# Kernel tuning notes

Measured on AMD Instinct MI355X. Metric: run time of the kernel, lower is better.

The kernel has to match this reference:

```python
import jax, jax.numpy as jnp
import numpy as np

B, S, D = 2, 2048, 4096
NH, NKV, HD = 32, 8, 128
NREP = NH // NKV

def setup_inputs() -> dict:
    key = jax.random.key(0)
    ks = jax.random.split(key, 7)
    sd = 0.02
    return {
        "x": jax.random.normal(ks[0], (B, S, D), dtype=jnp.float32),
        "freqs_cos": jnp.cos(jnp.outer(jnp.arange(S, dtype=jnp.float32), 1.0 / (10000.0 ** (jnp.arange(0, HD, 2, dtype=jnp.float32) / HD)))),
        "freqs_sin": jnp.sin(jnp.outer(jnp.arange(S, dtype=jnp.float32), 1.0 / (10000.0 ** (jnp.arange(0, HD, 2, dtype=jnp.float32) / HD)))),
        "wq": jax.random.normal(ks[1], (D, NH * HD), dtype=jnp.float32) * sd,
        "wk": jax.random.normal(ks[2], (D, NKV * HD), dtype=jnp.float32) * sd,
        "wv": jax.random.normal(ks[3], (D, NKV * HD), dtype=jnp.float32) * sd,
        "wo": jax.random.normal(ks[4], (NH * HD, D), dtype=jnp.float32) * sd,
    }

def _rope(t, cos, sin):
    # t: [b, s, h, hd]; cos/sin: [s, hd/2]
    tr = t.reshape(*t.shape[:-1], -1, 2)
    r, i = tr[..., 0], tr[..., 1]
    c = cos[None, :, None, :]
    s = sin[None, :, None, :]
    out_r = r * c - i * s
    out_i = r * s + i * c
    return jnp.stack([out_r, out_i], axis=-1).reshape(t.shape)

def reference(x, freqs_cos, freqs_sin, wq, wk, wv, wo):
    b, s, _ = x.shape
    xq = (x @ wq).reshape(b, s, NH, HD)
    xk = (x @ wk).reshape(b, s, NKV, HD)
    xv = (x @ wv).reshape(b, s, NKV, HD)
    xq = _rope(xq, freqs_cos, freqs_sin)
    xk = _rope(xk, freqs_cos, freqs_sin)
    # GQA via grouped einsum (equivalent to repeat_kv + SDPA)
    q = xq.transpose(0, 2, 1, 3).reshape(b, NKV, NREP, s, HD)  # [b,g,r,s,d]
    k = xk.transpose(0, 2, 1, 3)  # [b,g,t,d]
    v = xv.transpose(0, 2, 1, 3)
    scale = 1.0 / jnp.sqrt(jnp.float32(HD))
    scores = jnp.einsum('bgrsd,bgtd->bgrst', q, k) * scale
    mask = jnp.where(jnp.triu(jnp.ones((s, s), dtype=bool), 1), -jnp.inf, 0.0).astype(scores.dtype)
    probs = jax.nn.softmax(scores + mask, axis=-1)
    out = jnp.einsum('bgrst,bgtd->bgrsd', probs, v)
    out = out.reshape(b, NH, s, HD).transpose(0, 2, 1, 3).reshape(b, s, NH * HD)
    return out @ wo
```

## Files before the change

kernel.cpp:

```cpp
#include <hip/hip_runtime.h>
#include <hip/hip_bf16.h>
#include <math.h>

typedef __bf16 bf16_t;
typedef __bf16 bf16x4 __attribute__((ext_vector_type(4)));
typedef __bf16 bf16x8 __attribute__((ext_vector_type(8)));
typedef float  f32x4  __attribute__((ext_vector_type(4)));

#define B_   2
#define S_   2048
#define D_   4096
#define NH_  32
#define NKV_ 8
#define HD_  128
#define NREP_ 4
#define QKVN 6144

static __device__ __forceinline__ void gload_lds16(const bf16_t* g, bf16_t* l) {
  __builtin_amdgcn_global_load_lds(
      (const __attribute__((address_space(1))) void*)g,
      (__attribute__((address_space(3))) void*)l, 16, 0, 0);
}

__global__ void convert_f32_bf16(const float* __restrict__ in, bf16_t* __restrict__ out,
                                 size_t n8) {
  size_t i = (size_t)blockIdx.x * blockDim.x + threadIdx.x;
  if (i >= n8) return;
  f32x4 a = *(const f32x4*)(in + i * 8);
  f32x4 b = *(const f32x4*)(in + i * 8 + 4);
  bf16x8 o;
  o[0] = (bf16_t)a[0]; o[1] = (bf16_t)a[1]; o[2] = (bf16_t)a[2]; o[3] = (bf16_t)a[3];
  o[4] = (bf16_t)b[0]; o[5] = (bf16_t)b[1]; o[6] = (bf16_t)b[2]; o[7] = (bf16_t)b[3];
  *(bf16x8*)(out + i * 8) = o;
}

__global__ void transpose_convert(const float* __restrict__ in, bf16_t* __restrict__ out,
                                  int R, int C) {
  __shared__ float tile[32][33];
  const int c0 = blockIdx.x * 32, r0 = blockIdx.y * 32;
  const int tc = threadIdx.x & 31, tr = threadIdx.x >> 5;
#pragma unroll
  for (int i = 0; i < 4; i++) {
    int r = tr + i * 8;
    tile[r][tc] = in[(size_t)(r0 + r) * C + c0 + tc];
  }
  __syncthreads();
#pragma unroll
  for (int i = 0; i < 4; i++) {
    int r = tr + i * 8;
    out[(size_t)(c0 + r) * R + r0 + tc] = (bf16_t)tile[tc][r];
  }
}

__global__ void transpose_v(const bf16_t* __restrict__ qkv, bf16_t* __restrict__ out) {
  __shared__ bf16_t tile[32][33];
  const int t0 = blockIdx.x * 32, d0 = blockIdx.y * 32;
  const int bg = blockIdx.z, b = bg / NKV_, g = bg % NKV_;
  const bf16_t* ibase = qkv + (size_t)b * S_ * QKVN + 5120 + g * HD_;
  bf16_t* obase = out + ((size_t)b * NKV_ + g) * (size_t)HD_ * S_;
  const int tc = threadIdx.x & 31, tr = threadIdx.x >> 5;
#pragma unroll
  for (int i = 0; i < 4; i++) {
    int t = t0 + tr + i * 8;
    tile[tr + i * 8][tc] = ibase[(size_t)t * QKVN + d0 + tc];
  }
  __syncthreads();
#pragma unroll
  for (int i = 0; i < 4; i++) {
    int d = d0 + tr + i * 8;
    obase[(size_t)d * S_ + t0 + tc] = tile[tc][tr + i * 8];
  }
}

__global__ void rope_inplace(bf16_t* __restrict__ x, const float* __restrict__ cosT,
                             const float* __restrict__ sinT, int lgh, size_t nchunks) {
  size_t i = (size_t)blockIdx.x * blockDim.x + threadIdx.x;
  if (i >= nchunks) return;
  const int d8 = (int)(i & 15);
  const int h = (int)((i >> 4) & ((1u << lgh) - 1));
  const size_t pos = i >> (4 + lgh);
  const int s = (int)(pos & (S_ - 1));
  bf16_t* p = x + pos * QKVN + h * HD_ + d8 * 8;
  bf16x8 v = *(bf16x8*)p;
  f32x4 c  = *(const f32x4*)(cosT + (size_t)s * 64 + d8 * 4);
  f32x4 sn = *(const f32x4*)(sinT + (size_t)s * 64 + d8 * 4);
  bf16x8 o;
#pragma unroll
  for (int j = 0; j < 4; j++) {
    float re = (float)v[2 * j], im = (float)v[2 * j + 1];
    o[2 * j]     = (bf16_t)(re * c[j] - im * sn[j]);
    o[2 * j + 1] = (bf16_t)(re * sn[j] + im * c[j]);
  }
  *(bf16x8*)p = o;
}

template <typename OutT>
__global__ __launch_bounds__(512, 2) void gemm_nt256(const bf16_t* __restrict__ A,
                                                     const bf16_t* __restrict__ Bt,
                                                     OutT* __restrict__ C,
                                                     int M, int N, int K) {
  extern __shared__ __align__(16) bf16_t lds[];
  const int t = threadIdx.x;
  const int w = t >> 6, l = t & 63;
  const int wm = w >> 2, wn = w & 3;
  const int lr = l & 15, lg = l >> 4;

  const int nbx = gridDim.x;
  const int nwg = nbx * gridDim.y;
  const int bid = blockIdx.y * nbx + blockIdx.x;
  const int cpx = nwg >> 3;
  const int sid = (bid & 7) * cpx + (bid >> 3);
  const int n0 = (sid % nbx) * 256;
  const int m0 = (sid / nbx) * 256;

  const int srow = t >> 2;
  const int colsw = ((t & 3) * 8) ^ (((t >> 2) & 3) << 3);
  const bf16_t* Asrc0 = A  + (size_t)(m0 + srow) * K + colsw;
  const bf16_t* Asrc1 = A  + (size_t)(m0 + 128 + srow) * K + colsw;
  const bf16_t* Bsrc0 = Bt + (size_t)(n0 + srow) * K + colsw;
  const bf16_t* Bsrc1 = Bt + (size_t)(n0 + 128 + srow) * K + colsw;

  f32x4 acc[8][4];
  const f32x4 zero = {0.f, 0.f, 0.f, 0.f};
#pragma unroll
  for (int m = 0; m < 8; m++)
#pragma unroll
    for (int n = 0; n < 4; n++) acc[m][n] = zero;

  const int fo = (lg * 8) ^ ((lr & 3) << 3);

  auto STAGE = [&](int buf, int k0) {
    bf16_t* dA = lds + buf * 16384;
    bf16_t* dB = dA + 8192;
    gload_lds16(Asrc0 + k0, dA + t * 8);
    gload_lds16(Asrc1 + k0, dA + 4096 + t * 8);
    gload_lds16(Bsrc0 + k0, dB + t * 8);
    gload_lds16(Bsrc1 + k0, dB + 4096 + t * 8);
  };

  auto COMPUTE = [&](int buf) {
    const bf16_t* pA = lds + buf * 16384;
    const bf16_t* pB = pA + 8192;
    bf16x8 af[8], bfr[4];
#pragma unroll
    for (int m = 0; m < 8; m++)
      af[m] = *(const bf16x8*)(pA + (wm * 128 + m * 16 + lr) * 32 + fo);
#pragma unroll
    for (int n = 0; n < 4; n++)
      bfr[n] = *(const bf16x8*)(pB + (wn * 64 + n * 16 + lr) * 32 + fo);
    __builtin_amdgcn_s_setprio(1);
#pragma unroll
    for (int m = 0; m < 8; m++)
#pragma unroll
      for (int n = 0; n < 4; n++)
        acc[m][n] = __builtin_amdgcn_mfma_f32_16x16x32_bf16(af[m], bfr[n], acc[m][n], 0, 0, 0);
    __builtin_amdgcn_s_setprio(0);
  };

  const int KT = K >> 5;

  STAGE(0, 0);
  STAGE(1, 32);
  STAGE(2, 64);
  asm volatile("s_waitcnt vmcnt(8)" ::: "memory");
  __builtin_amdgcn_s_barrier();
  __builtin_amdgcn_sched_barrier(0);

  int kt = 0;
  for (; kt < KT - 3; ++kt) {
    STAGE((kt + 3) & 3, (kt + 3) << 5);
    COMPUTE(kt & 3);
    asm volatile("s_waitcnt vmcnt(8)" ::: "memory");
    __builtin_amdgcn_s_barrier();
    __builtin_amdgcn_sched_barrier(0);
  }
  COMPUTE(kt & 3);
  asm volatile("s_waitcnt vmcnt(4)" ::: "memory");
  __builtin_amdgcn_s_barrier();
  __builtin_amdgcn_sched_barrier(0);
  ++kt;
  COMPUTE(kt & 3);
  asm volatile("s_waitcnt vmcnt(0)" ::: "memory");
  __builtin_amdgcn_s_barrier();
  __builtin_amdgcn_sched_barrier(0);
  ++kt;
  COMPUTE(kt & 3);

#pragma unroll
  for (int m = 0; m < 8; m++)
#pragma unroll
    for (int n = 0; n < 4; n++) {
      const int row = m0 + wm * 128 + m * 16 + lg * 4;
      const int col = n0 + wn * 64 + n * 16 + lr;
#pragma unroll
      for (int r = 0; r < 4; r++) C[(size_t)(row + r) * N + col] = (OutT)acc[m][n][r];
    }
}

#define QBLK 128
#define KVBLK 64
__global__ __launch_bounds__(256, 2) void flash_attn3(const bf16_t* __restrict__ QKV,
                                                      const bf16_t* __restrict__ Vt,
                                                      bf16_t* __restrict__ O) {
  const int pair = blockIdx.x;
  const int h = blockIdx.y, b = blockIdx.z;
  const int g = h >> 2;
  const int t = threadIdx.x, w = t >> 6, l = t & 63;
  const int lr = l & 15, lg = l >> 4;

  __shared__ __align__(16) char lds[49152];
  char* Ks = lds;
  char* Vs = lds + 16384;
  char* Ps = lds + 32768 + w * 4096;

  const float scale = 0.08838834764831845f;
  const int xm = (lr & 7) << 4;

  for (int phase = 0; phase < 2; phase++) {
    const int qtile = phase ? (15 - pair) : pair;
    const int q0 = qtile * QBLK;
    const int wq = q0 + w * 32;

    bf16x8 qreg[2][4];
#pragma unroll
    for (int qt = 0; qt < 2; qt++)
#pragma unroll
      for (int kk = 0; kk < 4; kk++) {
        bf16x8 v = *(const bf16x8*)&QKV[((size_t)b * S_ + wq + qt * 16 + lr) * QKVN +
                                        h * HD_ + kk * 32 + lg * 8];
#pragma unroll
        for (int j = 0; j < 8; j++) v[j] = (bf16_t)((float)v[j] * scale);
        qreg[qt][kk] = v;
      }

    float mrun[2] = {-INFINITY, -INFINITY};
    float lrun[2] = {0.f, 0.f};
    f32x4 acc[2][8];
    const f32x4 zero = {0.f, 0.f, 0.f, 0.f};
#pragma unroll
    for (int qt = 0; qt < 2; qt++)
#pragma unroll
      for (int d = 0; d < 8; d++) acc[qt][d] = zero;

    const int nkb = (q0 + QBLK) >> 6;
    for (int kb = 0; kb < nkb; kb++) {
      const int t0 = kb * KVBLK;
      __syncthreads();
#pragma unroll
      for (int i = 0; i < 4; i++) {
        const int c = t + i * 256;
        const int row = c >> 4, sl = c & 15;
        bf16x8 kv = *(const bf16x8*)&QKV[((size_t)b * S_ + t0 + row) * QKVN + 4096 +
                                         g * HD_ + sl * 8];
        *(bf16x8*)(Ks + row * 256 + ((sl * 16) ^ ((row & 7) << 4))) = kv;
      }
#pragma unroll
      for (int i = 0; i < 4; i++) {
        const int c = t + i * 256;
        const int row = c >> 3, sl = c & 7;
        bf16x8 vv = *(const bf16x8*)&Vt[(((size_t)b * NKV_ + g) * HD_ + row) * S_ + t0 + sl * 8];
        *(bf16x8*)(Vs + row * 128 + ((sl * 16) ^ ((row & 7) << 4))) = vv;
      }
      __syncthreads();

      if (t0 > wq + 31) continue;

      f32x4 st[4][2];
#pragma unroll
      for (int n = 0; n < 4; n++) { st[n][0] = zero; st[n][1] = zero; }
#pragma unroll
      for (int kk = 0; kk < 4; kk++) {
        const int colb = (kk * 64 + lg * 16) ^ xm;
#pragma unroll
        for (int n = 0; n < 4; n++) {
          const bf16x8 ak = *(const bf16x8*)(Ks + (n * 16 + lr) * 256 + colb);
          st[n][0] = __builtin_amdgcn_mfma_f32_16x16x32_bf16(ak, qreg[0][kk], st[n][0], 0, 0, 0);
          st[n][1] = __builtin_amdgcn_mfma_f32_16x16x32_bf16(ak, qreg[1][kk], st[n][1], 0, 0, 0);
        }
      }

      const bool needmask = (t0 + KVBLK - 1 > wq);
#pragma unroll
      for (int qt = 0; qt < 2; qt++) {
        const int q = wq + qt * 16 + lr;
        if (needmask) {
#pragma unroll
          for (int n = 0; n < 4; n++)
#pragma unroll
            for (int r = 0; r < 4; r++)
              if (t0 + n * 16 + lg * 4 + r > q) st[n][qt][r] = -INFINITY;
        }
        float mx = -INFINITY;
#pragma unroll
        for (int n = 0; n < 4; n++)
#pragma unroll
          for (int r = 0; r < 4; r++) mx = fmaxf(mx, st[n][qt][r]);
        mx = fmaxf(mx, __shfl_xor(mx, 16));
        mx = fmaxf(mx, __shfl_xor(mx, 32));
        const float mnew = fmaxf(mrun[qt], mx);
        const float corr = __expf(mrun[qt] - mnew);
        mrun[qt] = mnew;
        float sum = 0.f;
        bf16x4 pk[4];
#pragma unroll
        for (int n = 0; n < 4; n++) {
#pragma unroll
          for (int r = 0; r < 4; r++) {
            const float p = __expf(st[n][qt][r] - mnew);
            sum += p;
            pk[n][r] = (bf16_t)p;
          }
        }
        sum += __shfl_xor(sum, 16);
        sum += __shfl_xor(sum, 32);
        lrun[qt] = lrun[qt] * corr + sum;
        {
          char* pbase = Ps + (qt * 16 + lr) * 128;
#pragma unroll
          for (int n = 0; n < 4; n++)
            *(bf16x4*)(pbase + ((n * 32 + lg * 8) ^ xm)) = pk[n];
        }
#pragma unroll
        for (int r = 0; r < 4; r++) {
          const float cb = __shfl(corr, lg * 4 + r);
#pragma unroll
          for (int db = 0; db < 8; db++) acc[qt][db][r] *= cb;
        }
      }

#pragma unroll
      for (int kk = 0; kk < 2; kk++) {
        const int colb = (kk * 64 + lg * 16) ^ xm;
        const bf16x8 ap0 = *(const bf16x8*)(Ps + lr * 128 + colb);
        const bf16x8 ap1 = *(const bf16x8*)(Ps + (16 + lr) * 128 + colb);
#pragma unroll
        for (int db = 0; db < 8; db++) {
          const bf16x8 bv = *(const bf16x8*)(Vs + (db * 16 + lr) * 128 + colb);
          acc[0][db] = __builtin_amdgcn_mfma_f32_16x16x32_bf16(ap0, bv, acc[0][db], 0, 0, 0);
          acc[1][db] = __builtin_amdgcn_mfma_f32_16x16x32_bf16(ap1, bv, acc[1][db], 0, 0, 0);
        }
      }
    }

#pragma unroll
    for (int qt = 0; qt < 2; qt++) {
      const float linv = 1.f / lrun[qt];
#pragma unroll
      for (int r = 0; r < 4; r++) {
        const float li = __shfl(linv, lg * 4 + r);
        const int q = wq + qt * 16 + lg * 4 + r;
#pragma unroll
        for (int db = 0; db < 8; db++)
          O[(((size_t)b * S_ + q) * NH_ + h) * HD_ + db * 16 + lr] = (bf16_t)(acc[qt][db][r] * li);
      }
    }
    __syncthreads();
  }
}

extern "C" void kernel_launch(void* const* d_in, const int* in_sizes, int n_in,
                              void* d_out, int out_size, void* d_ws, size_t ws_size,
                              hipStream_t stream) {
  const float* x    = (const float*)d_in[0];
  const float* fcos = (const float*)d_in[1];
  const float* fsin = (const float*)d_in[2];
  const float* wq   = (const float*)d_in[3];
  const float* wk   = (const float*)d_in[4];
  const float* wv   = (const float*)d_in[5];
  const float* wo   = (const float*)d_in[6];
  float* out = (float*)d_out;

  char* ws = (char*)d_ws;
  bf16_t* x_bf   = (bf16_t*)(ws);
  bf16_t* wqkvT  = (bf16_t*)(ws + 33554432);
  bf16_t* qkv    = (bf16_t*)(ws + 83886080);
  bf16_t* vt     = (bf16_t*)(ws + 134217728);
  bf16_t* attn   = (bf16_t*)(ws + 142606336);

  hipFuncSetAttribute(reinterpret_cast<const void*>(gemm_nt256<bf16_t>),
                      hipFuncAttributeMaxDynamicSharedMemorySize, 131072);
  hipFuncSetAttribute(reinterpret_cast<const void*>(gemm_nt256<float>),
                      hipFuncAttributeMaxDynamicSharedMemorySize, 131072);

  convert_f32_bf16<<<8192, 256, 0, stream>>>(x, x_bf, (size_t)2097152);
  transpose_convert<<<dim3(128, 128), 256, 0, stream>>>(wq, wqkvT, 4096, 4096);
  transpose_convert<<<dim3(32, 128), 256, 0, stream>>>(wk, wqkvT + (size_t)4096 * 4096, 4096, 1024);
  transpose_convert<<<dim3(32, 128), 256, 0, stream>>>(wv, wqkvT + (size_t)5120 * 4096, 4096, 1024);
  gemm_nt256<bf16_t><<<dim3(24, 16), 512, 131072, stream>>>(x_bf, wqkvT, qkv, 4096, QKVN, 4096);
  rope_inplace<<<8192, 256, 0, stream>>>(qkv, fcos, fsin, 5, (size_t)2097152);
  rope_inplace<<<2048, 256, 0, stream>>>(qkv + 4096, fcos, fsin, 3, (size_t)524288);
  transpose_v<<<dim3(64, 4, 16), 256, 0, stream>>>(qkv, vt);
  transpose_convert<<<dim3(128, 128), 256, 0, stream>>>(wo, wqkvT, 4096, 4096);
  flash_attn3<<<dim3(8, 32, 2), 256, 0, stream>>>(qkv, vt, attn);
  gemm_nt256<float><<<dim3(16, 16), 512, 131072, stream>>>(attn, wqkvT, out, 4096, 4096, 4096);
}
```

Baseline: 546.8 us.

## Restructure GEMM mainloop into 8-phase ping-pong with K=64 tiles

Replaces the 4-stage K=32 LDS ring in the bf16 GEMM with a double-buffered K=64 tile, split into four phases per iteration. Each phase interleaves LDS fragment reads, a slice of global-to-LDS staging for upcoming tiles, barriers and a group of MFMAs. The LDS swizzle moves to an 8-chunk XOR pattern. The aim is to overlap memory traffic with MFMA work more finely and reduce stalls. In exchange it adds more barriers per tile, and the buffer-reuse timing is tight.

```diff
diff --git a/kernel.cpp b/kernel.cpp
--- a/kernel.cpp
+++ b/kernel.cpp
@@ -95,10 +95,10 @@
 }
 
 template <typename OutT>
-__global__ __launch_bounds__(512, 2) void gemm_nt256(const bf16_t* __restrict__ A,
-                                                     const bf16_t* __restrict__ Bt,
-                                                     OutT* __restrict__ C,
-                                                     int M, int N, int K) {
+__global__ __launch_bounds__(512, 2) void gemm8p(const bf16_t* __restrict__ Ag,
+                                                 const bf16_t* __restrict__ Bg,
+                                                 OutT* __restrict__ C,
+                                                 int M, int N, int K) {
   extern __shared__ __align__(16) bf16_t lds[];
   const int t = threadIdx.x;
   const int w = t >> 6, l = t & 63;
@@ -113,12 +113,18 @@
   const int n0 = (sid % nbx) * 256;
   const int m0 = (sid / nbx) * 256;
 
-  const int srow = t >> 2;
-  const int colsw = ((t & 3) * 8) ^ (((t >> 2) & 3) << 3);
-  const bf16_t* Asrc0 = A  + (size_t)(m0 + srow) * K + colsw;
-  const bf16_t* Asrc1 = A  + (size_t)(m0 + 128 + srow) * K + colsw;
-  const bf16_t* Bsrc0 = Bt + (size_t)(n0 + srow) * K + colsw;
-  const bf16_t* Bsrc1 = Bt + (size_t)(n0 + 128 + srow) * K + colsw;
+  const int srow = t >> 3;
+  const int colsw = ((t & 7) ^ (srow & 7)) * 8;
+  const int xsw = (lr & 7) * 8;
+
+  auto stageA = [&](int db, int k0, int q) {
+    gload_lds16(Ag + (size_t)(m0 + q * 64 + srow) * K + k0 + colsw,
+                lds + db * 32768 + q * 4096 + t * 8);
+  };
+  auto stageB = [&](int db, int k0, int q) {
+    gload_lds16(Bg + (size_t)(n0 + q * 64 + srow) * K + k0 + colsw,
+                lds + db * 32768 + 16384 + q * 4096 + t * 8);
+  };
 
   f32x4 acc[8][4];
   const f32x4 zero = {0.f, 0.f, 0.f, 0.f};
@@ -127,64 +133,74 @@
 #pragma unroll
     for (int n = 0; n < 4; n++) acc[m][n] = zero;
 
-  const int fo = (lg * 8) ^ ((lr & 3) << 3);
-
-  auto STAGE = [&](int buf, int k0) {
-    bf16_t* dA = lds + buf * 16384;
-    bf16_t* dB = dA + 8192;
-    gload_lds16(Asrc0 + k0, dA + t * 8);
-    gload_lds16(Asrc1 + k0, dA + 4096 + t * 8);
-    gload_lds16(Bsrc0 + k0, dB + t * 8);
-    gload_lds16(Bsrc1 + k0, dB + 4096 + t * 8);
-  };
-
-  auto COMPUTE = [&](int buf) {
-    const bf16_t* pA = lds + buf * 16384;
-    const bf16_t* pB = pA + 8192;
-    bf16x8 af[8], bfr[4];
-#pragma unroll
-    for (int m = 0; m < 8; m++)
-      af[m] = *(const bf16x8*)(pA + (wm * 128 + m * 16 + lr) * 32 + fo);
-#pragma unroll
-    for (int n = 0; n < 4; n++)
-      bfr[n] = *(const bf16x8*)(pB + (wn * 64 + n * 16 + lr) * 32 + fo);
-    __builtin_amdgcn_s_setprio(1);
-#pragma unroll
-    for (int m = 0; m < 8; m++)
-#pragma unroll
-      for (int n = 0; n < 4; n++)
-        acc[m][n] = __builtin_amdgcn_mfma_f32_16x16x32_bf16(af[m], bfr[n], acc[m][n], 0, 0, 0);
-    __builtin_amdgcn_s_setprio(0);
-  };
-
-  const int KT = K >> 5;
-
-  STAGE(0, 0);
-  STAGE(1, 32);
-  STAGE(2, 64);
-  asm volatile("s_waitcnt vmcnt(8)" ::: "memory");
+  const int KT = K >> 6;
+
+#pragma unroll
+  for (int q = 0; q < 4; q++) stageA(0, 0, q);
+#pragma unroll
+  for (int q = 0; q < 4; q++) stageB(0, 0, q);
+#pragma unroll
+  for (int q = 0; q < 4; q++) stageB(1, 64, q);
+  stageA(1, 64, 0);
+  stageA(1, 64, 2);
+  asm volatile("s_waitcnt vmcnt(6)" ::: "memory");
   __builtin_amdgcn_s_barrier();
-  __builtin_amdgcn_sched_barrier(0);
-
-  int kt = 0;
-  for (; kt < KT - 3; ++kt) {
-    STAGE((kt + 3) & 3, (kt + 3) << 5);
-    COMPUTE(kt & 3);
-    asm volatile("s_waitcnt vmcnt(8)" ::: "memory");
-    __builtin_amdgcn_s_barrier();
-    __builtin_amdgcn_sched_barrier(0);
-  }
-  COMPUTE(kt & 3);
-  asm volatile("s_waitcnt vmcnt(4)" ::: "memory");
-  __builtin_amdgcn_s_barrier();
-  __builtin_amdgcn_sched_barrier(0);
-  ++kt;
-  COMPUTE(kt & 3);
-  asm volatile("s_waitcnt vmcnt(0)" ::: "memory");
-  __builtin_amdgcn_s_barrier();
-  __builtin_amdgcn_sched_barrier(0);
-  ++kt;
-  COMPUTE(kt & 3);
+
+  for (int c = 0; c < KT; ++c) {
+    const int d = c & 1;
+    const bf16_t* pA = lds + d * 32768;
+    const bf16_t* pB = pA + 16384;
+    const bool st2 = (c + 2) < KT;
+    const int k2 = (c + 2) << 6;
+    bf16x8 bfrag[4][2];
+
+#pragma unroll
+    for (int p = 0; p < 4; ++p) {
+      if (p == 0) {
+#pragma unroll
+        for (int n = 0; n < 4; n++)
+#pragma unroll
+          for (int ks = 0; ks < 2; ks++)
+            bfrag[n][ks] =
+                *(const bf16x8*)(pB + (wn * 64 + n * 16 + lr) * 64 + ((ks * 32 + lg * 8) ^ xsw));
+      }
+      bf16x8 a0 = *(const bf16x8*)(pA + (wm * 128 + (2 * p) * 16 + lr) * 64 + ((lg * 8) ^ xsw));
+      bf16x8 a1 = *(const bf16x8*)(pA + (wm * 128 + (2 * p) * 16 + lr) * 64 + ((32 + lg * 8) ^ xsw));
+      bf16x8 a2 = *(const bf16x8*)(pA + (wm * 128 + (2 * p + 1) * 16 + lr) * 64 + ((lg * 8) ^ xsw));
+      bf16x8 a3 = *(const bf16x8*)(pA + (wm * 128 + (2 * p + 1) * 16 + lr) * 64 + ((32 + lg * 8) ^ xsw));
+
+      if (p == 0) {
+        if (c + 1 < KT) { stageA(1 - d, (c + 1) << 6, 1); stageA(1 - d, (c + 1) << 6, 3); }
+      } else if (p == 1) {
+        if (st2) { stageB(d, k2, 0); stageB(d, k2, 1); }
+      } else if (p == 2) {
+        if (st2) { stageB(d, k2, 2); stageB(d, k2, 3); }
+      } else {
+        if (st2) { stageA(d, k2, 0); stageA(d, k2, 2); }
+      }
+
+      if (p == 0) asm volatile("s_waitcnt lgkmcnt(8)" ::: "memory");
+      __builtin_amdgcn_s_barrier();
+      asm volatile("s_waitcnt lgkmcnt(0)" ::: "memory");
+      __builtin_amdgcn_sched_barrier(0);
+
+      __builtin_amdgcn_s_setprio(1);
+#pragma unroll
+      for (int n = 0; n < 4; n++) {
+        acc[2 * p][n]     = __builtin_amdgcn_mfma_f32_16x16x32_bf16(a0, bfrag[n][0], acc[2 * p][n], 0, 0, 0);
+        acc[2 * p][n]     = __builtin_amdgcn_mfma_f32_16x16x32_bf16(a1, bfrag[n][1], acc[2 * p][n], 0, 0, 0);
+        acc[2 * p + 1][n] = __builtin_amdgcn_mfma_f32_16x16x32_bf16(a2, bfrag[n][0], acc[2 * p + 1][n], 0, 0, 0);
+        acc[2 * p + 1][n] = __builtin_amdgcn_mfma_f32_16x16x32_bf16(a3, bfrag[n][1], acc[2 * p + 1][n], 0, 0, 0);
+      }
+      __builtin_amdgcn_s_setprio(0);
+
+      if (p == 3) {
+        if (st2) asm volatile("s_waitcnt vmcnt(6)" ::: "memory");
+        else     asm volatile("s_waitcnt vmcnt(0)" ::: "memory");
+      }
+      __builtin_amdgcn_s_barrier();
+    }
+  }
 
 #pragma unroll
   for (int m = 0; m < 8; m++)
@@ -377,20 +393,20 @@
   bf16_t* vt     = (bf16_t*)(ws + 134217728);
   bf16_t* attn   = (bf16_t*)(ws + 142606336);
 
-  hipFuncSetAttribute(reinterpret_cast<const void*>(gemm_nt256<bf16_t>),
+  hipFuncSetAttribute(reinterpret_cast<const void*>(gemm8p<bf16_t>),
                       hipFuncAttributeMaxDynamicSharedMemorySize, 131072);
-  hipFuncSetAttribute(reinterpret_cast<const void*>(gemm_nt256<float>),
+  hipFuncSetAttribute(reinterpret_cast<const void*>(gemm8p<float>),
                       hipFuncAttributeMaxDynamicSharedMemorySize, 131072);
 
   convert_f32_bf16<<<8192, 256, 0, stream>>>(x, x_bf, (size_t)2097152);
   transpose_convert<<<dim3(128, 128), 256, 0, stream>>>(wq, wqkvT, 4096, 4096);
   transpose_convert<<<dim3(32, 128), 256, 0, stream>>>(wk, wqkvT + (size_t)4096 * 4096, 4096, 1024);
   transpose_convert<<<dim3(32, 128), 256, 0, stream>>>(wv, wqkvT + (size_t)5120 * 4096, 4096, 1024);
-  gemm_nt256<bf16_t><<<dim3(24, 16), 512, 131072, stream>>>(x_bf, wqkvT, qkv, 4096, QKVN, 4096);
+  gemm8p<bf16_t><<<dim3(24, 16), 512, 131072, stream>>>(x_bf, wqkvT, qkv, 4096, QKVN, 4096);
   rope_inplace<<<8192, 256, 0, stream>>>(qkv, fcos, fsin, 5, (size_t)2097152);
   rope_inplace<<<2048, 256, 0, stream>>>(qkv + 4096, fcos, fsin, 3, (size_t)524288);
   transpose_v<<<dim3(64, 4, 16), 256, 0, stream>>>(qkv, vt);
   transpose_convert<<<dim3(128, 128), 256, 0, stream>>>(wo, wqkvT, 4096, 4096);
   flash_attn3<<<dim3(8, 32, 2), 256, 0, stream>>>(qkv, vt, attn);
-  gemm_nt256<float><<<dim3(16, 16), 512, 131072, stream>>>(attn, wqkvT, out, 4096, 4096, 4096);
-}
+  gemm8p<float><<<dim3(16, 16), 512, 131072, stream>>>(attn, wqkvT, out, 4096, 4096, 4096);
+}
```

New measurement: 530.9 us. 2.9% less time.
